# Kernel tuning notes

Measured on AMD Instinct MI355X. Metric: run time of the kernel, lower is better.

## Reference

```python
import jax, jax.numpy as jnp
import numpy as np

N = 9
CELLS = N * N  # 81
B = 1024
HID = 100
EMPTY_P = 0.3


def _build_constraint_mask():
    # (81, 3, 81): mask[q, g, k] = 1 if cell k is in the same row/col/box as cell q
    m = np.zeros((CELLS, 3, CELLS), np.float32)
    for q in range(CELLS):
        r, c = divmod(q, N)
        for k in range(CELLS):
            r2, c2 = divmod(k, N)
            if r2 == r:
                m[q, 0, k] = 1.0
            if c2 == c:
                m[q, 1, k] = 1.0
            if (r2 // 3 == r // 3) and (c2 // 3 == c // 3):
                m[q, 2, k] = 1.0
    return jnp.asarray(m)


def setup_inputs() -> dict:
    key = jax.random.key(0)
    k1, k2, k3, k4 = jax.random.split(key, 4)
    # partially-filled boards: one-hot digits, ~EMPTY_P of cells zeroed (empty)
    digits = jax.random.randint(k1, (B, CELLS), 0, N)
    onehot = jax.nn.one_hot(digits, N, dtype=jnp.float32)
    filled = (jax.random.uniform(k2, (B, CELLS)) > EMPTY_P).astype(jnp.float32)
    x = onehot * filled[..., None]
    W1 = jax.random.normal(k3, (HID, 3 * N), dtype=jnp.float32) * 0.1
    W2 = jax.random.normal(k4, (N, HID), dtype=jnp.float32) * 0.1
    c = _build_constraint_mask()
    return {"x": x, "c": c, "W1": W1, "W2": W2}


def reference(x, c, W1, W2):
    bts = x.shape[0]
    # min_empty: max number of empty cells over the batch (fixed loop count, as in torch)
    T = int(jnp.max(jnp.sum(x.sum(axis=2) == 0, axis=1)))
    bidx = jnp.arange(bts)

    def step(carry, _):
        xc, xp = carry
        # constraints[b,q,g,d] = sum_k xc[b,k,d] * c[q,g,k]  (sparse graph aggregation)
        cons = jnp.einsum('bkd,qgk->bqgd', xc, c).reshape(bts, CELLS, 3 * N)
        empty = xc.sum(axis=2) == 0  # (B, 81)
        # masked MLP: compute everywhere, use only where empty (same math)
        y = jax.nn.relu(cons @ W1.T) @ W2.T  # (B, 81, 9)
        s_ = jax.nn.softmax(y, axis=-1)
        xp = jnp.where(empty[..., None], s_, xp)
        s = jnp.where(empty[..., None], s_, 0.0)
        score = s.max(axis=2)           # (B, 81)
        score_pos = s.argmax(axis=2)    # (B, 81)
        mmax = score.argmax(axis=1)     # (B,) most confident empty cell per board
        digit = score_pos[bidx, mmax]   # (B,)
        new_x = xc.at[bidx, mmax, digit].set(1.0)
        has_empty = empty.any(axis=1)
        xc = jnp.where(has_empty[:, None, None], new_x, xc)
        return (xc, xp), None

    (x_final, x_pred), _ = jax.lax.scan(step, (x, x), None, length=T)
    return (x_pred, x_final)
```

## Files before the change

### kernel.cpp

```cpp
#include <hip/hip_runtime.h>

#define CELLS 81
#define ND 9
#define HID 100
#define NP 52
#define PPW 13
#define NREG 8

typedef float v2f __attribute__((ext_vector_type(2)));

#define W1P_SZ (9 * NP * 8)
#define W2P_OFF W1P_SZ
#define W2P_SZ (NP * 20)
#define CNT_OFF (W2P_OFF + W2P_SZ)
#define ORD_OFF (CNT_OFF + 2)
#define BIGSLOTS 64
#define SPILLSLOTS 8
#define NBLK (BIGSLOTS + 512 + SPILLSLOTS)

__global__ __launch_bounds__(64) void prep_kernel(
    const float* __restrict__ x_all,
    const float* __restrict__ W1, const float* __restrict__ W2,
    float* __restrict__ ws, int* __restrict__ cnts, int* __restrict__ order,
    int nBoards)
{
    const int b = blockIdx.x, t = threadIdx.x;
    const int gid = b * 64 + t;

    if (gid < W1P_SZ) {
        int i = gid >> 3, k = gid & 7;
        int d = i / NP, j = i - d * NP;
        float v = 0.f;
        if (j < 50 && k < 6) {
            int u = 2 * j + (k & 1);
            v = W1[u*27 + (k >> 1) * 9 + d];
        }
        ws[gid] = v;
    } else if (gid < CNT_OFF) {
        int f = gid - W2P_OFF;
        int j = f / 20, k = f - j * 20;
        float v = 0.f;
        if (j < 50 && k < 18) {
            int d = k >> 1, u = 2 * j + (k & 1);
            v = W2[d*HID + u];
        }
        ws[gid] = v;
    }

    if (b >= nBoards) return;

    const float* xb = x_all + (size_t)b * (CELLS * ND);
    float mx = 0.f;
    #pragma unroll
    for (int d = 0; d < ND; ++d) mx = fmaxf(mx, xb[t*ND + d]);
    bool e1 = (mx < 0.5f);
    bool e2 = false;
    if (t < CELLS - 64) {
        float m2 = 0.f;
        #pragma unroll
        for (int d = 0; d < ND; ++d) m2 = fmaxf(m2, xb[(64+t)*ND + d]);
        e2 = (m2 < 0.5f);
    }
    unsigned long long m1 = __ballot(e1), m2b = __ballot(e2);
    if (t == 0) {
        int ne = __popcll(m1) + __popcll(m2b);
        if (ne > 32) {
            int p = atomicAdd(&cnts[0], 1) + 1;
            int blk = (p < BIGSLOTS) ? p : (BIGSLOTS + 512 + (p - BIGSLOTS));
            if (blk < NBLK) { order[2*blk] = b; order[2*blk + 1] = b; }
        } else {
            int p = atomicAdd(&cnts[1], 1) + 1;
            int blk = BIGSLOTS + (p >> 1);
            order[2*blk + (p & 1)] = b;
        }
    }
}

__global__ __launch_bounds__(256, 2) void sudoku_kernel(
    const float* __restrict__ x_all,
    const float* __restrict__ ws,
    const int* __restrict__ order,
    float* __restrict__ out, int nBoards)
{
    const int tid = threadIdx.x;
    const int wv  = tid >> 6;
    const int lw  = tid & 63;
    const int h   = lw >> 5;
    const int jbase = wv * PPW;

    const int s0  = order[2 * blockIdx.x];
    const int s1r = order[2 * blockIdx.x + 1];
    if (s0 < 0) return;
    const int s1 = (s1r < 0) ? s0 : s1r;
    const bool joined = (s0 == s1);
    const int myBoard = h ? s1 : s0;
    const int idx = joined ? 0 : h;

    float* pom = out + (size_t)myBoard * (CELLS * ND);

    __shared__ __align__(16) float w1s[W1P_SZ];
    __shared__ __align__(16) float w2s[W2P_SZ];
    __shared__ float parts[2][4][ND][64];
    __shared__ float cnt[2][3 * 81];
    __shared__ int   digit[2][CELLS];

    for (int i = tid; i < W1P_SZ / 4; i += 256)
        ((float4*)w1s)[i] = ((const float4*)ws)[i];
    for (int i = tid; i < W2P_SZ / 4; i += 256)
        ((float4*)w2s)[i] = ((const float4*)(ws + W2P_OFF))[i];
    for (int i = tid; i < 2 * 243; i += 256) (&cnt[0][0])[i] = 0.f;
    __syncthreads();

    float w2reg[NREG][18];
    #pragma unroll
    for (int j = 0; j < NREG; ++j) {
        const float* qq = &w2s[(jbase + j) * 20];
        #pragma unroll
        for (int k = 0; k < 18; ++k) w2reg[j][k] = qq[k];
    }

    {
        const int slot = (tid < 128) ? 0 : 1;
        const int t = (tid < 128) ? tid : tid - 128;
        const bool doSlot = (slot == 0) || !joined;
        const int bd = slot ? s1 : s0;
        const float* xb = x_all + (size_t)bd * (CELLS * ND);
        float* pob = out + (size_t)bd * (CELLS * ND);
        if (doSlot) {
            if (t < CELLS) {
                int dig = -1;
                #pragma unroll
                for (int d = 0; d < ND; ++d)
                    if (dig < 0 && xb[t*ND + d] > 0.5f) dig = d;
                digit[slot][t] = dig;
                if (dig >= 0) {
                    int r = t/9, c = t%9, b = (r/3)*3 + c/3;
                    atomicAdd(&cnt[slot][r*9 + dig], 1.f);
                    atomicAdd(&cnt[slot][81 + c*9 + dig], 1.f);
                    atomicAdd(&cnt[slot][162 + b*9 + dig], 1.f);
                }
            }
            for (int i = t; i < CELLS * ND; i += 128) pob[i] = xb[i];
        }
    }
    __syncthreads();

    const int rank = joined ? lw : (lw & 31);
    int myq = 127;
    int ne0 = 0, ne1 = 0;
    for (int q = 0; q < CELLS; ++q)
        if (digit[0][q] < 0) { if (idx == 0 && ne0 == rank) myq = q; ++ne0; }
    if (!joined) {
        for (int q = 0; q < CELLS; ++q)
            if (digit[1][q] < 0) { if (idx == 1 && ne1 == rank) myq = q; ++ne1; }
    } else ne1 = ne0;
    if (ne0 > 64) ne0 = 64;
    if (ne1 > 64) ne1 = 64;
    const int ne_mine = idx ? ne1 : ne0;
    const int itMax = max(ne0, ne1);
    bool active = (rank < ne_mine);

    const int myr = (myq < 81) ? myq / 9 : 0;
    const int myc = (myq < 81) ? myq % 9 : 0;
    const int myb = (myr / 3) * 3 + myc / 3;

    float crr[9], ccc[9], cbb[9];
    #pragma unroll
    for (int j = 0; j < 9; ++j) {
        crr[j] = cnt[idx][myr*9 + j];
        ccc[j] = cnt[idx][81 + myc*9 + j];
        cbb[j] = cnt[idx][162 + myb*9 + j];
    }
    v2f z2[PPW];
    #pragma unroll
    for (int j = 0; j < PPW; ++j) {
        v2f a = (v2f){0.f, 0.f};
        #pragma unroll
        for (int d = 0; d < 9; ++d) {
            const float* p = &w1s[(d*NP + jbase + j) * 8];
            float4 ab = *(const float4*)p;
            v2f Cv = *(const v2f*)(p + 4);
            v2f Av = (v2f){ab.x, ab.y}, Bv = (v2f){ab.z, ab.w};
            a += crr[d]*Av + ccc[d]*Bv + cbb[d]*Cv;
        }
        z2[j] = a;
    }

    int dc = 0;
    v2f b0v = (v2f){0.f,0.f}, b1v = (v2f){0.f,0.f}, b2v = (v2f){0.f,0.f};
    float pfin[ND];

    for (int it = 0; it < itMax; ++it) {
        const float* w1r = &w1s[(dc*NP + jbase) * 8];
        const float* w2r = &w2s[jbase * 20];

        v2f acc2[ND];
        #pragma unroll
        for (int d = 0; d < ND; ++d) acc2[d] = (v2f){0.f, 0.f};

        #pragma unroll
        for (int j = 0; j < PPW; ++j) {
            const float* p = w1r + j*8;
            float4 ab = *(const float4*)p;
            v2f Cv = *(const v2f*)(p + 4);
            v2f Av = (v2f){ab.x, ab.y}, Bv = (v2f){ab.z, ab.w};
            v2f zv = z2[j];
            zv = b0v*Av + (b1v*Bv + (b2v*Cv + zv));
            z2[j] = zv;
            v2f hh;
            hh.x = fmaxf(zv.x, 0.f);
            hh.y = fmaxf(zv.y, 0.f);
            if (j < NREG) {
                #pragma unroll
                for (int d = 0; d < ND; ++d)
                    acc2[d] += hh * (v2f){w2reg[j][2*d], w2reg[j][2*d + 1]};
            } else {
                const float* qq = w2r + j*20;
                float4 w01 = *(const float4*)qq;
                float4 w23 = *(const float4*)(qq + 4);
                float4 w45 = *(const float4*)(qq + 8);
                float4 w67 = *(const float4*)(qq + 12);
                v2f w8 = *(const v2f*)(qq + 16);
                acc2[0] += hh * (v2f){w01.x, w01.y};
                acc2[1] += hh * (v2f){w01.z, w01.w};
                acc2[2] += hh * (v2f){w23.x, w23.y};
                acc2[3] += hh * (v2f){w23.z, w23.w};
                acc2[4] += hh * (v2f){w45.x, w45.y};
                acc2[5] += hh * (v2f){w45.z, w45.w};
                acc2[6] += hh * (v2f){w67.x, w67.y};
                acc2[7] += hh * (v2f){w67.z, w67.w};
                acc2[8] += hh * w8;
            }
        }

        const int buf = it & 1;
        #pragma unroll
        for (int d = 0; d < ND; ++d)
            parts[buf][wv][d][lw] = acc2[d].x + acc2[d].y;
        __syncthreads();

        float acc[ND];
        #pragma unroll
        for (int d = 0; d < ND; ++d) acc[d] = parts[buf][0][d][lw];
        #pragma unroll
        for (int ow = 1; ow < 4; ++ow) {
            #pragma unroll
            for (int d = 0; d < ND; ++d) acc[d] += parts[buf][ow][d][lw];
        }

        float m9 = fmaxf(fmaxf(fmaxf(acc[0],acc[1]), fmaxf(acc[2],acc[3])),
                         fmaxf(fmaxf(acc[4],acc[5]), fmaxf(acc[6],acc[7])));
        m9 = fmaxf(m9, acc[8]);
        float s = 0.f;
        #pragma unroll
        for (int d = 0; d < ND; ++d) { acc[d] = __expf(acc[d] - m9); s += acc[d]; }
        float inv = 1.f / s;
        float bv = -1.f; int bd = 0;
        #pragma unroll
        for (int d = 0; d < ND; ++d) {
            acc[d] *= inv;
            if (acc[d] > bv) { bv = acc[d]; bd = d; }
        }

        float bvv = active ? bv : -1.f;
        float vmax = bvv;
        #pragma unroll
        for (int off = 16; off >= 1; off >>= 1)
            vmax = fmaxf(vmax, __shfl_xor(vmax, off));
        if (joined) vmax = fmaxf(vmax, __shfl_xor(vmax, 32));
        const unsigned long long segMask =
            joined ? ~0ull : (h ? 0xFFFFFFFF00000000ull : 0x00000000FFFFFFFFull);
        unsigned long long msk = __ballot(active && (bvv == vmax)) & segMask;
        const bool valid = (msk != 0);
        int wl = valid ? (__ffsll(msk) - 1) : 0;
        int qw = __shfl(myq, wl);
        int dwn = __shfl(bd, wl);

        if (active && valid && myq == qw) {
            #pragma unroll
            for (int d = 0; d < ND; ++d) pfin[d] = acc[d];
            if (wv == 0) digit[idx][myq] = dwn;
            active = false;
        }
        const int pr = qw/9, pcc = qw%9, pb = (pr/3)*3 + pcc/3;
        b0v = (v2f)((valid && myr == pr)  ? 1.f : 0.f);
        b1v = (v2f)((valid && myc == pcc) ? 1.f : 0.f);
        b2v = (v2f)((valid && myb == pb)  ? 1.f : 0.f);
        if (valid) dc = dwn;
    }

    __syncthreads();
    if (wv == 0 && myq < 81) {
        #pragma unroll
        for (int d = 0; d < ND; ++d) pom[myq*ND + d] = pfin[d];
    }
    {
        const int slot = (tid < 128) ? 0 : 1;
        const int t = (tid < 128) ? tid : tid - 128;
        const bool doSlot = (slot == 0) || !joined;
        const int bd2 = slot ? s1 : s0;
        float* fob = out + (size_t)nBoards * (CELLS * ND) + (size_t)bd2 * (CELLS * ND);
        if (doSlot) {
            for (int i = t; i < CELLS * ND; i += 128) {
                int q = i / ND, d = i - q * ND;
                fob[i] = (digit[slot][q] == d) ? 1.f : 0.f;
            }
        }
    }
}

extern "C" void kernel_launch(void* const* d_in, const int* in_sizes, int n_in,
                              void* d_out, int out_size, void* d_ws, size_t ws_size,
                              hipStream_t stream) {
    const float* x  = (const float*)d_in[0];
    const float* W1 = (const float*)d_in[2];
    const float* W2 = (const float*)d_in[3];
    float* out = (float*)d_out;
    float* ws  = (float*)d_ws;
    int nBoards = in_sizes[0] / (CELLS * ND);
    int* cnts   = (int*)ws + CNT_OFF;
    int* ordArr = (int*)ws + ORD_OFF;
    hipMemsetAsync(cnts, 0xFF, (2 + 2 * NBLK) * sizeof(int), stream);
    prep_kernel<<<nBoards, 64, 0, stream>>>(x, W1, W2, ws, cnts, ordArr, nBoards);
    sudoku_kernel<<<NBLK, 256, 0, stream>>>(x, ws, ordArr, out, nBoards);
}
```

Baseline: 147.5 us.

## Sort boards by empty-cell count via bucket histogram for longest-first scheduling

Replaces the two-class (big/small) board ordering with a 65-bucket histogram of empty-cell counts, then a single-block scatter kernel builds a block order sorted in descending empty count. Big boards still get one block each and small boards are paired, but now the longest boards launch first. The goal is to cut tail imbalance, since the loop length per board depends on its empty count. It adds an extra kernel launch and a serial prefix scan, and changes the grid size to nBoards.

```diff
diff --git a/kernel.cpp b/kernel.cpp
--- a/kernel.cpp
+++ b/kernel.cpp
@@ -12,16 +12,14 @@
 #define W1P_SZ (9 * NP * 8)
 #define W2P_OFF W1P_SZ
 #define W2P_SZ (NP * 20)
-#define CNT_OFF (W2P_OFF + W2P_SZ)
-#define ORD_OFF (CNT_OFF + 2)
-#define BIGSLOTS 64
-#define SPILLSLOTS 8
-#define NBLK (BIGSLOTS + 512 + SPILLSLOTS)
+#define BCNT_OFF (W2P_OFF + W2P_SZ)
+#define ORD_OFF (BCNT_OFF + 65)
+#define SLOT_OFF (ORD_OFF + 2048)
 
 __global__ __launch_bounds__(64) void prep_kernel(
     const float* __restrict__ x_all,
     const float* __restrict__ W1, const float* __restrict__ W2,
-    float* __restrict__ ws, int* __restrict__ cnts, int* __restrict__ order,
+    float* __restrict__ ws, int* __restrict__ bcnt, int* __restrict__ slot,
     int nBoards)
 {
     const int b = blockIdx.x, t = threadIdx.x;
@@ -36,7 +34,7 @@
             v = W1[u*27 + (k >> 1) * 9 + d];
         }
         ws[gid] = v;
-    } else if (gid < CNT_OFF) {
+    } else if (gid < BCNT_OFF) {
         int f = gid - W2P_OFF;
         int j = f / 20, k = f - j * 20;
         float v = 0.f;
@@ -64,14 +62,45 @@
     unsigned long long m1 = __ballot(e1), m2b = __ballot(e2);
     if (t == 0) {
         int ne = __popcll(m1) + __popcll(m2b);
-        if (ne > 32) {
-            int p = atomicAdd(&cnts[0], 1) + 1;
-            int blk = (p < BIGSLOTS) ? p : (BIGSLOTS + 512 + (p - BIGSLOTS));
-            if (blk < NBLK) { order[2*blk] = b; order[2*blk + 1] = b; }
-        } else {
-            int p = atomicAdd(&cnts[1], 1) + 1;
-            int blk = BIGSLOTS + (p >> 1);
-            order[2*blk + (p & 1)] = b;
+        if (ne > 64) ne = 64;
+        int r = atomicAdd(&bcnt[ne], 1) + 1;
+        if (r < 256) slot[ne * 256 + r] = b;
+    }
+}
+
+__global__ __launch_bounds__(256) void scatter_kernel(
+    const int* __restrict__ bcnt, const int* __restrict__ slot,
+    int* __restrict__ order)
+{
+    __shared__ int base[66];
+    __shared__ int cntS[65];
+    __shared__ int nBigS;
+    const int t = threadIdx.x;
+    if (t < 65) cntS[t] = bcnt[t] + 1;
+    __syncthreads();
+    if (t == 0) {
+        int acc = 0, nb = 0;
+        for (int ne = 64; ne >= 0; --ne) {
+            base[ne] = acc;
+            acc += cntS[ne];
+            if (ne > 32) nb += cntS[ne];
+        }
+        nBigS = nb;
+    }
+    __syncthreads();
+    const int nBig = nBigS;
+    for (int ne = 64; ne >= 0; --ne) {
+        const int c = cntS[ne];
+        for (int r = t; r < c; r += 256) {
+            int board = slot[ne * 256 + r];
+            int pos = base[ne] + r;
+            if (ne > 32) {
+                order[2*pos] = board; order[2*pos + 1] = board;
+            } else {
+                int rr = pos - nBig;
+                int blk = nBig + (rr >> 1);
+                order[2*blk + (rr & 1)] = board;
+            }
         }
     }
 }
@@ -318,9 +347,11 @@
     float* out = (float*)d_out;
     float* ws  = (float*)d_ws;
     int nBoards = in_sizes[0] / (CELLS * ND);
-    int* cnts   = (int*)ws + CNT_OFF;
+    int* bcnt   = (int*)ws + BCNT_OFF;
     int* ordArr = (int*)ws + ORD_OFF;
-    hipMemsetAsync(cnts, 0xFF, (2 + 2 * NBLK) * sizeof(int), stream);
-    prep_kernel<<<nBoards, 64, 0, stream>>>(x, W1, W2, ws, cnts, ordArr, nBoards);
-    sudoku_kernel<<<NBLK, 256, 0, stream>>>(x, ws, ordArr, out, nBoards);
+    int* slot   = (int*)ws + SLOT_OFF;
+    hipMemsetAsync(bcnt, 0xFF, (65 + 2048) * sizeof(int), stream);
+    prep_kernel<<<nBoards, 64, 0, stream>>>(x, W1, W2, ws, bcnt, slot, nBoards);
+    scatter_kernel<<<1, 256, 0, stream>>>(bcnt, slot, ordArr);
+    sudoku_kernel<<<nBoards, 256, 0, stream>>>(x, ws, ordArr, out, nBoards);
 }
```

After: 135.8 us. 8.0% less time.
